# Kernel optimization log

Hardware: AMD Instinct MI355X
Metric: run time of the kernel (lower is better)

The kernel has to match this reference:

```python
import jax, jax.numpy as jnp
import numpy as np

N, E, IN, HID, HEADS, L = 50000, 640000, 32, 64, 2, 4
MAXR = 8
N_ETYPE = 11 + 3 * MAXR  # 35
NEG_SLOPE = 0.2  # DGL EGATConv leaky_relu slope


def _mlp2(x, W1, b1, W2, b2):
    # 2-layer MLP: activation (gelu) after hidden layer only
    return jax.nn.gelu(x @ W1 + b1) @ W2 + b2


def _egat(h, ef, src, dst, W_ni, W_nj, W_fij, W_node, b_node, attn):
    # DGL EGATConv: edge-feature-enhanced graph attention
    n = h.shape[0]
    H, D = attn.shape
    f_edge = (h @ W_ni)[src] + (h @ W_nj)[dst] + ef @ W_fij       # [E, H*D]
    f_out = jax.nn.leaky_relu(f_edge, NEG_SLOPE).reshape(-1, H, D)
    e = jnp.einsum('ehd,hd->eh', f_out, attn)                     # [E, H]
    m = jax.ops.segment_max(e, dst, num_segments=n)               # per-dst max
    w = jnp.exp(e - m[dst])
    z = jax.ops.segment_sum(w, dst, num_segments=n)
    a = w / z[dst]                                                # edge softmax over incoming edges
    h_out = (h @ W_node + b_node).reshape(n, H, D)
    return jax.ops.segment_sum(h_out[src] * a[:, :, None], dst, num_segments=n)  # [N, H, D]


def _forward(feat, att_rc, att_rp, type_emb, rid_emb, rc_W, rc_b, rp_W, rp_b,
             fe_W1, fe_b1, fe_W2, fe_b2, W_ni, W_nj, W_fij, W_node, b_node, attn,
             mlp_W1, mlp_b1, mlp_W2, mlp_b2, src, dst, etype, erid):
    n = feat.shape[0]
    # edge embedding, 'sum' flavor
    ef = type_emb[etype] + rid_emb[erid] + att_rc @ rc_W + rc_b + att_rp @ rp_W + rp_b
    feats = [feat]
    h = _mlp2(feat, fe_W1, fe_b1, fe_W2, fe_b2)
    feats.append(h)
    for l in range(W_ni.shape[0]):
        agg = _egat(h, ef, src, dst, W_ni[l], W_nj[l], W_fij[l],
                    W_node[l], b_node[l], attn[l])
        h = _mlp2(agg.reshape(n, -1), mlp_W1[l], mlp_b1[l], mlp_W2[l], mlp_b2[l]) + h  # residual
        feats.append(h)
    node_emb = jnp.concatenate(feats, axis=-1)             # layer_pooling='all'
    graph_emb = jnp.max(node_emb, axis=0, keepdims=True)   # graph max pooling
    return jnp.concatenate([node_emb, jnp.broadcast_to(graph_emb, node_emb.shape)], axis=-1)


def setup_inputs() -> dict:
    key = jax.random.key(0)
    ks = iter(jax.random.split(key, 40))
    s = 0.05
    return {
        'feat': jax.random.normal(next(ks), (N, IN), jnp.float32),
        'att_rc': jax.random.normal(next(ks), (E, 2), jnp.float32),
        'att_rp': jax.random.normal(next(ks), (E, 3), jnp.float32),
        'type_emb': jax.random.normal(next(ks), (N_ETYPE, HID), jnp.float32) * s,
        'rid_emb': jax.random.normal(next(ks), (MAXR + 1, HID), jnp.float32) * s,
        'rc_W': jax.random.normal(next(ks), (2, HID), jnp.float32) * s,
        'rc_b': jnp.zeros((HID,), jnp.float32),
        'rp_W': jax.random.normal(next(ks), (3, HID), jnp.float32) * s,
        'rp_b': jnp.zeros((HID,), jnp.float32),
        'fe_W1': jax.random.normal(next(ks), (IN, HID), jnp.float32) * s,
        'fe_b1': jnp.zeros((HID,), jnp.float32),
        'fe_W2': jax.random.normal(next(ks), (HID, HID), jnp.float32) * s,
        'fe_b2': jnp.zeros((HID,), jnp.float32),
        'W_ni': jax.random.normal(next(ks), (L, HID, HEADS * HID), jnp.float32) * s,
        'W_nj': jax.random.normal(next(ks), (L, HID, HEADS * HID), jnp.float32) * s,
        'W_fij': jax.random.normal(next(ks), (L, HID, HEADS * HID), jnp.float32) * s,
        'W_node': jax.random.normal(next(ks), (L, HID, HEADS * HID), jnp.float32) * s,
        'b_node': jnp.zeros((L, HEADS * HID), jnp.float32),
        'attn': jax.random.normal(next(ks), (L, HEADS, HID), jnp.float32) * s,
        'mlp_W1': jax.random.normal(next(ks), (L, HEADS * HID, HEADS * HID), jnp.float32) * s,
        'mlp_b1': jnp.zeros((L, HEADS * HID), jnp.float32),
        'mlp_W2': jax.random.normal(next(ks), (L, HEADS * HID, HID), jnp.float32) * s,
        'mlp_b2': jnp.zeros((L, HID), jnp.float32),
        'src': jax.random.randint(next(ks), (E,), 0, N, jnp.int32),
        'dst': jax.random.randint(next(ks), (E,), 0, N, jnp.int32),
        'etype': jax.random.randint(next(ks), (E,), 0, N_ETYPE, jnp.int32),
        'erid': jax.random.randint(next(ks), (E,), 0, MAXR + 1, jnp.int32),
    }


def reference(feat, att_rc, att_rp, type_emb, rid_emb, rc_W, rc_b, rp_W, rp_b,
              fe_W1, fe_b1, fe_W2, fe_b2, W_ni, W_nj, W_fij, W_node, b_node, attn,
              mlp_W1, mlp_b1, mlp_W2, mlp_b2, src, dst, etype, erid):
    return _forward(feat, att_rc, att_rp, type_emb, rid_emb, rc_W, rc_b, rp_W, rp_b,
                    fe_W1, fe_b1, fe_W2, fe_b2, W_ni, W_nj, W_fij, W_node, b_node, attn,
                    mlp_W1, mlp_b1, mlp_W2, mlp_b2, src, dst, etype, erid)
```

## Files before the change

### kernel.cpp

```cpp
#include <hip/hip_runtime.h>
#include <math.h>

#define N_NODES 50000
#define N_EDGES 640000
#define NLAYER  4
#define NPAD    50016

typedef unsigned short bf16_t;
typedef __attribute__((ext_vector_type(8))) short s16x8;
typedef __attribute__((ext_vector_type(4))) float f32x4;

__device__ __forceinline__ float gelu_f(float x) {
    return 0.5f * x * (1.0f + tanhf(0.7978845608028654f * (x + 0.044715f * x * x * x)));
}

__device__ __forceinline__ bf16_t f2bf(float f) {
    unsigned u = __float_as_uint(f);
    unsigned r = (u + 0x7FFFu + ((u >> 16) & 1u)) >> 16;
    return (bf16_t)r;
}
__device__ __forceinline__ float bf2f(bf16_t h) { return __uint_as_float(((unsigned)h) << 16); }
__device__ __forceinline__ float bfl(unsigned x) { return __uint_as_float(x << 16); }
__device__ __forceinline__ float bfh(unsigned x) { return __uint_as_float(x & 0xFFFF0000u); }

__global__ void k_zero32(unsigned* p, int n) {
    int i = blockIdx.x * 256 + threadIdx.x;
    if (i < n) p[i] = 0u;
}

__global__ void k_hist(const int* __restrict__ dst, int* __restrict__ deg) {
    int i = blockIdx.x * 256 + threadIdx.x;
    if (i < N_EDGES) atomicAdd(&deg[dst[i]], 1);
}

__global__ void k_scan1(const int* __restrict__ deg, int* __restrict__ rowptr, int* __restrict__ bsum) {
    __shared__ int sd[1024];
    int gi = blockIdx.x * 1024 + threadIdx.x;
    int v = (gi < N_NODES) ? deg[gi] : 0;
    sd[threadIdx.x] = v;
    __syncthreads();
    for (int off = 1; off < 1024; off <<= 1) {
        int t2 = (threadIdx.x >= (unsigned)off) ? sd[threadIdx.x - off] : 0;
        __syncthreads();
        sd[threadIdx.x] += t2;
        __syncthreads();
    }
    if (gi < N_NODES) rowptr[gi] = sd[threadIdx.x] - v;
    if (threadIdx.x == 1023) bsum[blockIdx.x] = sd[1023];
}

__global__ void k_scan2(const int* __restrict__ bsum, int* __restrict__ boff, int nb) {
    if (threadIdx.x == 0 && blockIdx.x == 0) {
        int run = 0;
        for (int b = 0; b < nb; b++) { boff[b] = run; run += bsum[b]; }
    }
}

__global__ void k_scan3(int* __restrict__ rowptr, const int* __restrict__ boff) {
    int gi = blockIdx.x * 1024 + threadIdx.x;
    if (gi < N_NODES) rowptr[gi] += boff[blockIdx.x];
    if (gi == 0) rowptr[N_NODES] = N_EDGES;
}

__global__ void k_copy(const int* __restrict__ a, int* __restrict__ b) {
    int i = blockIdx.x * 256 + threadIdx.x;
    if (i < N_NODES) b[i] = a[i];
}

__global__ void k_scatter(const int* __restrict__ dst, int* __restrict__ cursor, int* __restrict__ eidx) {
    int i = blockIdx.x * 256 + threadIdx.x;
    if (i < N_EDGES) {
        int p = atomicAdd(&cursor[dst[i]], 1);
        eidx[p] = i;
    }
}

__global__ void k_sortgather(
    const int* __restrict__ eidx, const int* __restrict__ src, const int* __restrict__ dst,
    const int* __restrict__ etype, const int* __restrict__ erid,
    const float* __restrict__ att_rc, const float* __restrict__ att_rp,
    int* __restrict__ src_s, int* __restrict__ dst_s,
    int* __restrict__ etype_s, int* __restrict__ erid_s,
    float* __restrict__ rc_s, float* __restrict__ rp_s)
{
    int i = blockIdx.x * 256 + threadIdx.x;
    if (i < N_EDGES) {
        int e = eidx[i];
        src_s[i] = src[e];
        dst_s[i] = dst[e];
        etype_s[i] = etype[e];
        erid_s[i] = erid[e];
        rc_s[2 * i] = att_rc[2 * e];
        rc_s[2 * i + 1] = att_rc[2 * e + 1];
        rp_s[3 * i] = att_rp[3 * e];
        rp_s[3 * i + 1] = att_rp[3 * e + 1];
        rp_s[3 * i + 2] = att_rp[3 * e + 2];
    }
}

__global__ void k_wprep(const float* __restrict__ Wfij, const float* __restrict__ Wni,
                        const float* __restrict__ Wnj, const float* __restrict__ Wnode,
                        const float* __restrict__ W1, const float* __restrict__ W2,
                        bf16_t* __restrict__ WT, bf16_t* __restrict__ W3T,
                        bf16_t* __restrict__ W1T, bf16_t* __restrict__ W2T)
{
    int idx = blockIdx.x * 256 + threadIdx.x;
    if (idx >= NLAYER * 57344) return;
    int l = idx / 57344, r = idx % 57344;
    if (r < 8192) {
        int n = r >> 6, k = r & 63;
        WT[l * 8192 + r] = f2bf(Wfij[l * 8192 + k * 128 + n]);
    } else if (r < 32768) {
        int q = r - 8192; int c = q >> 6, k = q & 63;
        const float* src = (c < 128) ? Wni : (c < 256) ? Wnj : Wnode;
        W3T[l * 24576 + q] = f2bf(src[l * 8192 + k * 128 + (c & 127)]);
    } else if (r < 49152) {
        int q = r - 32768; int n = q >> 7, k = q & 127;
        W1T[l * 16384 + q] = f2bf(W1[l * 16384 + k * 128 + n]);
    } else {
        int q = r - 49152; int j = q >> 7, k = q & 127;
        W2T[l * 8192 + q] = f2bf(W2[l * 8192 + k * 64 + j]);
    }
}

__global__ __launch_bounds__(256) void k_fe(
    const float* __restrict__ feat, const float* __restrict__ W1, const float* __restrict__ b1,
    const float* __restrict__ W2, const float* __restrict__ b2,
    float* __restrict__ h, bf16_t* __restrict__ hb, float* __restrict__ out)
{
    __shared__ float hid[4][64];
    int w = threadIdx.x >> 6, lane = threadIdx.x & 63;
    int n = blockIdx.x * 4 + w;
    float a = b1[lane];
#pragma unroll 8
    for (int k = 0; k < 32; k++) a = fmaf(feat[n * 32 + k], W1[k * 64 + lane], a);
    hid[w][lane] = gelu_f(a);
    __syncthreads();
    float o = b2[lane];
#pragma unroll 8
    for (int k = 0; k < 64; k++) o = fmaf(hid[w][k], W2[k * 64 + lane], o);
    h[n * 64 + lane] = o;
    hb[n * 64 + lane] = f2bf(o);
    out[n * 704 + 32 + lane] = o;
    if (lane < 32) out[n * 704 + lane] = feat[n * 32 + lane];
}

__global__ __launch_bounds__(256) void k_node3(
    const bf16_t* __restrict__ hb, const bf16_t* __restrict__ W3T,
    const float* __restrict__ bnode, bf16_t* __restrict__ s)
{
    __shared__ __align__(16) bf16_t hbS[32 * 72];
    const int t = threadIdx.x;
    const int wave = t >> 6, lane = t & 63, l16 = lane & 15, quad = lane >> 4;
    const int n0 = blockIdx.x * 32;
    {
        int r = t >> 3, sg = t & 7;
        *(s16x8*)(hbS + r * 72 + sg * 8) = *(const s16x8*)(hb + (size_t)(n0 + r) * 64 + sg * 8);
    }
    __syncthreads();
    const int ng = wave & 1, ch = wave >> 1;
    const s16x8 B0 = *(const s16x8*)(hbS + (ng * 16 + l16) * 72 + quad * 8);
    const s16x8 B1 = *(const s16x8*)(hbS + (ng * 16 + l16) * 72 + 32 + quad * 8);
    const int node = n0 + ng * 16 + l16;
#pragma unroll
    for (int nt = 0; nt < 12; nt++) {
        int c0 = ch * 192 + nt * 16;
        const s16x8 A0 = *(const s16x8*)(W3T + (size_t)(c0 + l16) * 64 + quad * 8);
        const s16x8 A1 = *(const s16x8*)(W3T + (size_t)(c0 + l16) * 64 + 32 + quad * 8);
        f32x4 acc = {0.f, 0.f, 0.f, 0.f};
        acc = __builtin_amdgcn_mfma_f32_16x16x32_bf16(A0, B0, acc, 0, 0, 0);
        acc = __builtin_amdgcn_mfma_f32_16x16x32_bf16(A1, B1, acc, 0, 0, 0);
        int cb = c0 + quad * 4;
        float4 bv = make_float4(0.f, 0.f, 0.f, 0.f);
        if (cb >= 256) bv = *(const float4*)(bnode + cb - 256);
        ushort4 o;
        o.x = f2bf(acc[0] + bv.x);
        o.y = f2bf(acc[1] + bv.y);
        o.z = f2bf(acc[2] + bv.z);
        o.w = f2bf(acc[3] + bv.w);
        *(ushort4*)(s + (size_t)node * 384 + cb) = o;
    }
}

__global__ __launch_bounds__(256) void k_edge(
    const bf16_t* __restrict__ s, const bf16_t* __restrict__ WT,
    const float* __restrict__ attn,
    const float* __restrict__ type_emb, const float* __restrict__ rid_emb,
    const float* __restrict__ rcW, const float* __restrict__ rcb,
    const float* __restrict__ rpW, const float* __restrict__ rpb,
    const float* __restrict__ rc_s, const float* __restrict__ rp_s,
    const int* __restrict__ etype_s, const int* __restrict__ erid_s,
    const int* __restrict__ src_s, const int* __restrict__ dst_s,
    float* __restrict__ evals)
{
    __shared__ __align__(16) bf16_t efA[32 * 72];
    __shared__ __align__(16) bf16_t SND[32 * 136];
    const int t = threadIdx.x;
    const int wave = t >> 6, lane = t & 63;
    const int l16 = lane & 15, quad = lane >> 4;
    const int eg = wave & 1, head = wave >> 1;

    s16x8 Aw[4][2];
    float4 att4[4];
#pragma unroll
    for (int mt = 0; mt < 4; mt++) {
        const bf16_t* wrow = WT + (head * 64 + mt * 16 + l16) * 64 + quad * 8;
        Aw[mt][0] = *(const s16x8*)(wrow);
        Aw[mt][1] = *(const s16x8*)(wrow + 32);
        att4[mt] = *(const float4*)(attn + head * 64 + mt * 16 + quad * 4);
    }

    for (int tile = blockIdx.x; tile < N_EDGES / 32; tile += gridDim.x) {
        const int eb = tile * 32;
        __syncthreads();
        {
            int e = t & 31, kg = (t >> 5) * 8;
            int i = eb + e;
            int et = etype_s[i] * 64, er = erid_s[i] * 64;
            float rc0 = rc_s[i * 2 + 0], rc1 = rc_s[i * 2 + 1];
            float rp0 = rp_s[i * 3 + 0], rp1 = rp_s[i * 3 + 1], rp2 = rp_s[i * 3 + 2];
            bf16_t tmp[8];
#pragma unroll
            for (int kk = 0; kk < 8; kk++) {
                int k = kg + kk;
                float v = type_emb[et + k] + rid_emb[er + k] + rcb[k] + rpb[k];
                v = fmaf(rc0, rcW[k], v);
                v = fmaf(rc1, rcW[64 + k], v);
                v = fmaf(rp0, rpW[k], v);
                v = fmaf(rp1, rpW[64 + k], v);
                v = fmaf(rp2, rpW[128 + k], v);
                tmp[kk] = f2bf(v);
            }
            *(s16x8*)(&efA[e * 72 + kg]) = *(const s16x8*)tmp;
        }
        {
#pragma unroll
            for (int j = 0; j < 2; j++) {
                int c = t * 2 + j;
                int e = c >> 4, p = c & 15;
                int i = eb + e;
                const uint4 U = *(const uint4*)(s + (size_t)src_s[i] * 384 + p * 8);
                const uint4 V = *(const uint4*)(s + (size_t)dst_s[i] * 384 + 128 + p * 8);
                bf16_t o[8];
                o[0] = f2bf(bfl(U.x) + bfl(V.x)); o[1] = f2bf(bfh(U.x) + bfh(V.x));
                o[2] = f2bf(bfl(U.y) + bfl(V.y)); o[3] = f2bf(bfh(U.y) + bfh(V.y));
                o[4] = f2bf(bfl(U.z) + bfl(V.z)); o[5] = f2bf(bfh(U.z) + bfh(V.z));
                o[6] = f2bf(bfl(U.w) + bfl(V.w)); o[7] = f2bf(bfh(U.w) + bfh(V.w));
                *(s16x8*)(&SND[e * 136 + p * 8]) = *(const s16x8*)o;
            }
        }
        __syncthreads();

        const int e = eg * 16 + l16;
        const s16x8 B0 = *(const s16x8*)(&efA[e * 72 + quad * 8]);
        const s16x8 B1 = *(const s16x8*)(&efA[e * 72 + 32 + quad * 8]);
        f32x4 acc[4];
#pragma unroll
        for (int mt = 0; mt < 4; mt++) {
            f32x4 a = {0.f, 0.f, 0.f, 0.f};
            a = __builtin_amdgcn_mfma_f32_16x16x32_bf16(Aw[mt][0], B0, a, 0, 0, 0);
            a = __builtin_amdgcn_mfma_f32_16x16x32_bf16(Aw[mt][1], B1, a, 0, 0, 0);
            acc[mt] = a;
        }

        float p = 0.f;
#pragma unroll
        for (int mt = 0; mt < 4; mt++) {
            const ushort4 sv = *(const ushort4*)(&SND[e * 136 + mt * 16 + quad * 4]);
            float f0 = acc[mt][0] + bf2f(sv.x);
            float f1 = acc[mt][1] + bf2f(sv.y);
            float f2 = acc[mt][2] + bf2f(sv.z);
            float f3 = acc[mt][3] + bf2f(sv.w);
            f0 = (f0 >= 0.f) ? f0 : 0.2f * f0;
            f1 = (f1 >= 0.f) ? f1 : 0.2f * f1;
            f2 = (f2 >= 0.f) ? f2 : 0.2f * f2;
            f3 = (f3 >= 0.f) ? f3 : 0.2f * f3;
            p = fmaf(f0, att4[mt].x, p);
            p = fmaf(f1, att4[mt].y, p);
            p = fmaf(f2, att4[mt].z, p);
            p = fmaf(f3, att4[mt].w, p);
        }
        p += __shfl_xor(p, 16);
        p += __shfl_xor(p, 32);
        if (quad == 0) evals[(eb + e) * 2 + head] = p;
    }
}

__global__ __launch_bounds__(256) void k_soft_agg(
    const int* __restrict__ rowptr, const int* __restrict__ src_s,
    const float* __restrict__ evals, const bf16_t* __restrict__ s,
    unsigned* __restrict__ aggb)
{
    int lane = threadIdx.x & 63;
    int wid = (blockIdx.x * 256 + threadIdx.x) >> 6;
    int nw = (gridDim.x * 256) >> 6;
    const int h1 = (lane >= 32) ? 1 : 0;
    const int half = lane & 31;
    for (int n = wid; n < N_NODES; n += nw) {
        int r0 = rowptr[n], r1 = rowptr[n + 1];
        unsigned* aout = aggb + (size_t)n * 64 + lane;
        if (r0 == r1) { *aout = 0u; continue; }
        float mm = -1e30f;
        for (int i = r0 + half; i < r1; i += 32) mm = fmaxf(mm, evals[2 * i + h1]);
#pragma unroll
        for (int off = 1; off < 32; off <<= 1) mm = fmaxf(mm, __shfl_xor(mm, off));
        float z = 0.f;
        for (int i = r0 + half; i < r1; i += 32) z += expf(evals[2 * i + h1] - mm);
#pragma unroll
        for (int off = 1; off < 32; off <<= 1) z += __shfl_xor(z, off);
        float rz = 1.f / z;
        float acc0 = 0.f, acc1 = 0.f;
        for (int i = r0; i < r1; i += 8) {
            int cnt = r1 - i;
            unsigned cc[8]; float ww[8];
#pragma unroll
            for (int j = 0; j < 8; j++) {
                if (j < cnt) {
                    cc[j] = *(const unsigned*)(s + (size_t)src_s[i + j] * 384 + 256 + 2 * lane);
                    ww[j] = expf(evals[2 * (i + j) + h1] - mm) * rz;
                } else { cc[j] = 0u; ww[j] = 0.f; }
            }
#pragma unroll
            for (int j = 0; j < 8; j++) {
                acc0 = fmaf(ww[j], bfl(cc[j]), acc0);
                acc1 = fmaf(ww[j], bfh(cc[j]), acc1);
            }
        }
        *aout = (unsigned)f2bf(acc0) | ((unsigned)f2bf(acc1) << 16);
    }
}

__global__ __launch_bounds__(256) void k_mlp(
    const bf16_t* __restrict__ aggb, const bf16_t* __restrict__ W1T, const float* __restrict__ b1,
    const bf16_t* __restrict__ W2T, const float* __restrict__ b2,
    const float* __restrict__ hin, float* __restrict__ hout, bf16_t* __restrict__ houtb,
    float* __restrict__ out, int col0)
{
    __shared__ __align__(16) bf16_t aggS[32 * 136];
    __shared__ __align__(16) bf16_t hidS[32 * 136];
    const int t = threadIdx.x;
    const int wave = t >> 6, lane = t & 63, l16 = lane & 15, quad = lane >> 4;
    const int n0 = blockIdx.x * 32;
    {
        int r = t >> 3, sg = t & 7;
        *(s16x8*)(aggS + r * 136 + sg * 16) =
            *(const s16x8*)(aggb + (size_t)(n0 + r) * 128 + sg * 16);
        *(s16x8*)(aggS + r * 136 + sg * 16 + 8) =
            *(const s16x8*)(aggb + (size_t)(n0 + r) * 128 + sg * 16 + 8);
    }
    __syncthreads();
    const int ng = wave & 1, nh = wave >> 1;
    const int node = n0 + ng * 16 + l16;
    {
        const bf16_t* brow = aggS + (ng * 16 + l16) * 136 + quad * 8;
        s16x8 B[4];
#pragma unroll
        for (int ks = 0; ks < 4; ks++) B[ks] = *(const s16x8*)(brow + ks * 32);
#pragma unroll
        for (int nt = 0; nt < 4; nt++) {
            int nb = nh * 64 + nt * 16;
            f32x4 acc = {0.f, 0.f, 0.f, 0.f};
#pragma unroll
            for (int ks = 0; ks < 4; ks++) {
                const s16x8 A = *(const s16x8*)(W1T + (size_t)(nb + l16) * 128 + ks * 32 + quad * 8);
                acc = __builtin_amdgcn_mfma_f32_16x16x32_bf16(A, B[ks], acc, 0, 0, 0);
            }
            const float4 bv = *(const float4*)(b1 + nb + quad * 4);
            ushort4 o;
            o.x = f2bf(gelu_f(acc[0] + bv.x));
            o.y = f2bf(gelu_f(acc[1] + bv.y));
            o.z = f2bf(gelu_f(acc[2] + bv.z));
            o.w = f2bf(gelu_f(acc[3] + bv.w));
            *(ushort4*)(hidS + (ng * 16 + l16) * 136 + nb + quad * 4) = o;
        }
    }
    __syncthreads();
    {
        const int jh = wave >> 1;
        const bf16_t* hrow = hidS + (ng * 16 + l16) * 136 + quad * 8;
        s16x8 H[4];
#pragma unroll
        for (int ks = 0; ks < 4; ks++) H[ks] = *(const s16x8*)(hrow + ks * 32);
#pragma unroll
        for (int jt = 0; jt < 2; jt++) {
            int jb = jh * 32 + jt * 16;
            f32x4 acc = {0.f, 0.f, 0.f, 0.f};
#pragma unroll
            for (int ks = 0; ks < 4; ks++) {
                const s16x8 A = *(const s16x8*)(W2T + (size_t)(jb + l16) * 128 + ks * 32 + quad * 8);
                acc = __builtin_amdgcn_mfma_f32_16x16x32_bf16(A, H[ks], acc, 0, 0, 0);
            }
            int j0 = jb + quad * 4;
            const float4 bv = *(const float4*)(b2 + j0);
            const float4 hv = *(const float4*)(hin + (size_t)node * 64 + j0);
            float4 v;
            v.x = acc[0] + bv.x + hv.x;
            v.y = acc[1] + bv.y + hv.y;
            v.z = acc[2] + bv.z + hv.z;
            v.w = acc[3] + bv.w + hv.w;
            *(float4*)(hout + (size_t)node * 64 + j0) = v;
            ushort4 ob;
            ob.x = f2bf(v.x); ob.y = f2bf(v.y); ob.z = f2bf(v.z); ob.w = f2bf(v.w);
            *(ushort4*)(houtb + (size_t)node * 64 + j0) = ob;
            if (node < N_NODES)
                *(float4*)(out + (size_t)node * 704 + col0 + j0) = v;
        }
    }
}

__device__ __forceinline__ unsigned fmap(float v) {
    unsigned u = __float_as_uint(v);
    return (u & 0x80000000u) ? ~u : (u | 0x80000000u);
}

__global__ __launch_bounds__(384) void k_colmax(const float* __restrict__ out, unsigned* __restrict__ gmax) {
    int c = threadIdx.x;
    if (c >= 352) return;
    float m = -1e30f;
    for (int n = blockIdx.x; n < N_NODES; n += gridDim.x)
        m = fmaxf(m, out[(size_t)n * 704 + c]);
    atomicMax(gmax + c, fmap(m));
}

__global__ __launch_bounds__(384) void k_bcast(const unsigned* __restrict__ gmax, float* __restrict__ out) {
    int c = threadIdx.x;
    if (c >= 352) return;
    unsigned u = gmax[c];
    u = (u & 0x80000000u) ? (u ^ 0x80000000u) : ~u;
    float v = __uint_as_float(u);
    for (int n = blockIdx.x; n < N_NODES; n += gridDim.x)
        out[(size_t)n * 704 + 352 + c] = v;
}

extern "C" void kernel_launch(void* const* d_in, const int* in_sizes, int n_in,
                              void* d_out, int out_size, void* d_ws, size_t ws_size,
                              hipStream_t stream)
{
    (void)in_sizes; (void)n_in; (void)out_size; (void)ws_size;
    const float* feat     = (const float*)d_in[0];
    const float* att_rc   = (const float*)d_in[1];
    const float* att_rp   = (const float*)d_in[2];
    const float* type_emb = (const float*)d_in[3];
    const float* rid_emb  = (const float*)d_in[4];
    const float* rc_W     = (const float*)d_in[5];
    const float* rc_b     = (const float*)d_in[6];
    const float* rp_W     = (const float*)d_in[7];
    const float* rp_b     = (const float*)d_in[8];
    const float* fe_W1    = (const float*)d_in[9];
    const float* fe_b1    = (const float*)d_in[10];
    const float* fe_W2    = (const float*)d_in[11];
    const float* fe_b2    = (const float*)d_in[12];
    const float* W_ni     = (const float*)d_in[13];
    const float* W_nj     = (const float*)d_in[14];
    const float* W_fij    = (const float*)d_in[15];
    const float* W_node   = (const float*)d_in[16];
    const float* b_node   = (const float*)d_in[17];
    const float* attn     = (const float*)d_in[18];
    const float* mlp_W1   = (const float*)d_in[19];
    const float* mlp_b1   = (const float*)d_in[20];
    const float* mlp_W2   = (const float*)d_in[21];
    const float* mlp_b2   = (const float*)d_in[22];
    const int* src   = (const int*)d_in[23];
    const int* dst   = (const int*)d_in[24];
    const int* etype = (const int*)d_in[25];
    const int* erid  = (const int*)d_in[26];
    float* out = (float*)d_out;

    char* cur = (char*)d_ws;
    auto alloc = [&](size_t bytes) { char* p = cur; cur += (bytes + 15) & ~(size_t)15; return p; };
    float* h_a    = (float*)alloc((size_t)NPAD * 64 * 4);
    float* h_b    = (float*)alloc((size_t)NPAD * 64 * 4);
    bf16_t* hb_a  = (bf16_t*)alloc((size_t)NPAD * 64 * 2);
    bf16_t* hb_b  = (bf16_t*)alloc((size_t)NPAD * 64 * 2);
    bf16_t* s     = (bf16_t*)alloc((size_t)NPAD * 384 * 2);
    float* ev     = (float*)alloc((size_t)N_EDGES * 2 * 4);
    bf16_t* aggb  = (bf16_t*)alloc((size_t)NPAD * 128 * 2);
    int* deg     = (int*)alloc((size_t)N_NODES * 4);
    int* rowptr  = (int*)alloc((size_t)(N_NODES + 1) * 4);
    int* cursor  = (int*)alloc((size_t)N_NODES * 4);
    int* eidx    = (int*)alloc((size_t)N_EDGES * 4);
    int* src_s   = (int*)alloc((size_t)N_EDGES * 4);
    int* dst_s   = (int*)alloc((size_t)N_EDGES * 4);
    int* etype_s = (int*)alloc((size_t)N_EDGES * 4);
    int* erid_s  = (int*)alloc((size_t)N_EDGES * 4);
    float* rc_s  = (float*)alloc((size_t)N_EDGES * 2 * 4);
    float* rp_s  = (float*)alloc((size_t)N_EDGES * 3 * 4);
    bf16_t* WT   = (bf16_t*)alloc((size_t)NLAYER * 128 * 64 * 2);
    bf16_t* W3T  = (bf16_t*)alloc((size_t)NLAYER * 384 * 64 * 2);
    bf16_t* W1T  = (bf16_t*)alloc((size_t)NLAYER * 128 * 128 * 2);
    bf16_t* W2T  = (bf16_t*)alloc((size_t)NLAYER * 64 * 128 * 2);
    int* bsum    = (int*)alloc(64 * 4);
    int* boff    = (int*)alloc(64 * 4);
    unsigned* gmax = (unsigned*)alloc(352 * 4);

    const int NB = (N_NODES + 1023) / 1024;

    k_zero32<<<(N_NODES + 255) / 256, 256, 0, stream>>>((unsigned*)deg, N_NODES);
    k_zero32<<<2, 256, 0, stream>>>(gmax, 352);
    k_hist<<<N_EDGES / 256, 256, 0, stream>>>(dst, deg);
    k_scan1<<<NB, 1024, 0, stream>>>(deg, rowptr, bsum);
    k_scan2<<<1, 64, 0, stream>>>(bsum, boff, NB);
    k_scan3<<<NB, 1024, 0, stream>>>(rowptr, boff);
    k_copy<<<(N_NODES + 255) / 256, 256, 0, stream>>>(rowptr, cursor);
    k_scatter<<<N_EDGES / 256, 256, 0, stream>>>(dst, cursor, eidx);
    k_sortgather<<<N_EDGES / 256, 256, 0, stream>>>(eidx, src, dst, etype, erid, att_rc, att_rp,
                                                    src_s, dst_s, etype_s, erid_s, rc_s, rp_s);
    k_wprep<<<(NLAYER * 57344 + 255) / 256, 256, 0, stream>>>(
        W_fij, W_ni, W_nj, W_node, mlp_W1, mlp_W2, WT, W3T, W1T, W2T);
    k_fe<<<N_NODES / 4, 256, 0, stream>>>(feat, fe_W1, fe_b1, fe_W2, fe_b2, h_a, hb_a, out);

    float* hc = h_a;  bf16_t* hbc = hb_a;
    float* hn = h_b;  bf16_t* hbn = hb_b;
    for (int l = 0; l < NLAYER; l++) {
        k_node3<<<NPAD / 32, 256, 0, stream>>>(hbc, W3T + (size_t)l * 384 * 64, b_node + l * 128, s);
        k_edge<<<2560, 256, 0, stream>>>(s, WT + l * 128 * 64, attn + l * 128,
                                         type_emb, rid_emb, rc_W, rc_b, rp_W, rp_b,
                                         rc_s, rp_s, etype_s, erid_s, src_s, dst_s, ev);
        k_soft_agg<<<4096, 256, 0, stream>>>(rowptr, src_s, ev, s, (unsigned*)aggb);
        k_mlp<<<NPAD / 32, 256, 0, stream>>>(aggb, W1T + (size_t)l * 128 * 128, mlp_b1 + l * 128,
                                             W2T + (size_t)l * 64 * 128, mlp_b2 + l * 64,
                                             hc, hn, hbn, out, 32 + 64 * (l + 1));
        float* tf = hc; hc = hn; hn = tf;
        bf16_t* tb = hbc; hbc = hbn; hbn = tb;
    }
    k_colmax<<<512, 384, 0, stream>>>(out, gmax);
    k_bcast<<<512, 384, 0, stream>>>(gmax, out);
}
```

Before: 1.332 ms.

## Gather node projections into registers in edge kernel, one tile per block

Measured after the change: 1.729 ms. 1.3x slower.

```diff
diff --git a/kernel.cpp b/kernel.cpp
--- a/kernel.cpp
+++ b/kernel.cpp
@@ -194,11 +194,22 @@
     float* __restrict__ evals)
 {
     __shared__ __align__(16) bf16_t efA[32 * 72];
-    __shared__ __align__(16) bf16_t SND[32 * 136];
     const int t = threadIdx.x;
     const int wave = t >> 6, lane = t & 63;
     const int l16 = lane & 15, quad = lane >> 4;
     const int eg = wave & 1, head = wave >> 1;
+    const int eb = blockIdx.x * 32;
+    const int e = eg * 16 + l16;
+    const int gi = eb + e;
+
+    const int srcn = src_s[gi], dstn = dst_s[gi];
+    ushort4 u4[4], v4[4];
+#pragma unroll
+    for (int mt = 0; mt < 4; mt++) {
+        const int c = head * 64 + mt * 16 + quad * 4;
+        u4[mt] = *(const ushort4*)(s + (size_t)srcn * 384 + c);
+        v4[mt] = *(const ushort4*)(s + (size_t)dstn * 384 + 128 + c);
+    }
 
     s16x8 Aw[4][2];
     float4 att4[4];
@@ -210,80 +221,58 @@
         att4[mt] = *(const float4*)(attn + head * 64 + mt * 16 + quad * 4);
     }
 
-    for (int tile = blockIdx.x; tile < N_EDGES / 32; tile += gridDim.x) {
-        const int eb = tile * 32;
-        __syncthreads();
-        {
-            int e = t & 31, kg = (t >> 5) * 8;
-            int i = eb + e;
-            int et = etype_s[i] * 64, er = erid_s[i] * 64;
-            float rc0 = rc_s[i * 2 + 0], rc1 = rc_s[i * 2 + 1];
-            float rp0 = rp_s[i * 3 + 0], rp1 = rp_s[i * 3 + 1], rp2 = rp_s[i * 3 + 2];
-            bf16_t tmp[8];
-#pragma unroll
-            for (int kk = 0; kk < 8; kk++) {
-                int k = kg + kk;
-                float v = type_emb[et + k] + rid_emb[er + k] + rcb[k] + rpb[k];
-                v = fmaf(rc0, rcW[k], v);
-                v = fmaf(rc1, rcW[64 + k], v);
-                v = fmaf(rp0, rpW[k], v);
-                v = fmaf(rp1, rpW[64 + k], v);
-                v = fmaf(rp2, rpW[128 + k], v);
-                tmp[kk] = f2bf(v);
-            }
-            *(s16x8*)(&efA[e * 72 + kg]) = *(const s16x8*)tmp;
+    {
+        int el = t & 31, kg = (t >> 5) * 8;
+        int i = eb + el;
+        int et = etype_s[i] * 64, er = erid_s[i] * 64;
+        float rc0 = rc_s[i * 2 + 0], rc1 = rc_s[i * 2 + 1];
+        float rp0 = rp_s[i * 3 + 0], rp1 = rp_s[i * 3 + 1], rp2 = rp_s[i * 3 + 2];
+        bf16_t tmp[8];
+#pragma unroll
+        for (int kk = 0; kk < 8; kk++) {
+            int k = kg + kk;
+            float v = type_emb[et + k] + rid_emb[er + k] + rcb[k] + rpb[k];
+            v = fmaf(rc0, rcW[k], v);
+            v = fmaf(rc1, rcW[64 + k], v);
+            v = fmaf(rp0, rpW[k], v);
+            v = fmaf(rp1, rpW[64 + k], v);
+            v = fmaf(rp2, rpW[128 + k], v);
+            tmp[kk] = f2bf(v);
         }
-        {
-#pragma unroll
-            for (int j = 0; j < 2; j++) {
-                int c = t * 2 + j;
-                int e = c >> 4, p = c & 15;
-                int i = eb + e;
-                const uint4 U = *(const uint4*)(s + (size_t)src_s[i] * 384 + p * 8);
-                const uint4 V = *(const uint4*)(s + (size_t)dst_s[i] * 384 + 128 + p * 8);
-                bf16_t o[8];
-                o[0] = f2bf(bfl(U.x) + bfl(V.x)); o[1] = f2bf(bfh(U.x) + bfh(V.x));
-                o[2] = f2bf(bfl(U.y) + bfl(V.y)); o[3] = f2bf(bfh(U.y) + bfh(V.y));
-                o[4] = f2bf(bfl(U.z) + bfl(V.z)); o[5] = f2bf(bfh(U.z) + bfh(V.z));
-                o[6] = f2bf(bfl(U.w) + bfl(V.w)); o[7] = f2bf(bfh(U.w) + bfh(V.w));
-                *(s16x8*)(&SND[e * 136 + p * 8]) = *(const s16x8*)o;
-            }
-        }
-        __syncthreads();
-
-        const int e = eg * 16 + l16;
-        const s16x8 B0 = *(const s16x8*)(&efA[e * 72 + quad * 8]);
-        const s16x8 B1 = *(const s16x8*)(&efA[e * 72 + 32 + quad * 8]);
-        f32x4 acc[4];
-#pragma unroll
-        for (int mt = 0; mt < 4; mt++) {
-            f32x4 a = {0.f, 0.f, 0.f, 0.f};
-            a = __builtin_amdgcn_mfma_f32_16x16x32_bf16(Aw[mt][0], B0, a, 0, 0, 0);
-            a = __builtin_amdgcn_mfma_f32_16x16x32_bf16(Aw[mt][1], B1, a, 0, 0, 0);
-            acc[mt] = a;
-        }
-
-        float p = 0.f;
-#pragma unroll
-        for (int mt = 0; mt < 4; mt++) {
-            const ushort4 sv = *(const ushort4*)(&SND[e * 136 + mt * 16 + quad * 4]);
-            float f0 = acc[mt][0] + bf2f(sv.x);
-            float f1 = acc[mt][1] + bf2f(sv.y);
-            float f2 = acc[mt][2] + bf2f(sv.z);
-            float f3 = acc[mt][3] + bf2f(sv.w);
-            f0 = (f0 >= 0.f) ? f0 : 0.2f * f0;
-            f1 = (f1 >= 0.f) ? f1 : 0.2f * f1;
-            f2 = (f2 >= 0.f) ? f2 : 0.2f * f2;
-            f3 = (f3 >= 0.f) ? f3 : 0.2f * f3;
-            p = fmaf(f0, att4[mt].x, p);
-            p = fmaf(f1, att4[mt].y, p);
-            p = fmaf(f2, att4[mt].z, p);
-            p = fmaf(f3, att4[mt].w, p);
-        }
-        p += __shfl_xor(p, 16);
-        p += __shfl_xor(p, 32);
-        if (quad == 0) evals[(eb + e) * 2 + head] = p;
-    }
+        *(s16x8*)(&efA[el * 72 + kg]) = *(const s16x8*)tmp;
+    }
+    __syncthreads();
+
+    const s16x8 B0 = *(const s16x8*)(&efA[e * 72 + quad * 8]);
+    const s16x8 B1 = *(const s16x8*)(&efA[e * 72 + 32 + quad * 8]);
+    f32x4 acc[4];
+#pragma unroll
+    for (int mt = 0; mt < 4; mt++) {
+        f32x4 a = {0.f, 0.f, 0.f, 0.f};
+        a = __builtin_amdgcn_mfma_f32_16x16x32_bf16(Aw[mt][0], B0, a, 0, 0, 0);
+        a = __builtin_amdgcn_mfma_f32_16x16x32_bf16(Aw[mt][1], B1, a, 0, 0, 0);
+        acc[mt] = a;
+    }
+
+    float p = 0.f;
+#pragma unroll
+    for (int mt = 0; mt < 4; mt++) {
+        float f0 = acc[mt][0] + bf2f(u4[mt].x) + bf2f(v4[mt].x);
+        float f1 = acc[mt][1] + bf2f(u4[mt].y) + bf2f(v4[mt].y);
+        float f2 = acc[mt][2] + bf2f(u4[mt].z) + bf2f(v4[mt].z);
+        float f3 = acc[mt][3] + bf2f(u4[mt].w) + bf2f(v4[mt].w);
+        f0 = (f0 >= 0.f) ? f0 : 0.2f * f0;
+        f1 = (f1 >= 0.f) ? f1 : 0.2f * f1;
+        f2 = (f2 >= 0.f) ? f2 : 0.2f * f2;
+        f3 = (f3 >= 0.f) ? f3 : 0.2f * f3;
+        p = fmaf(f0, att4[mt].x, p);
+        p = fmaf(f1, att4[mt].y, p);
+        p = fmaf(f2, att4[mt].z, p);
+        p = fmaf(f3, att4[mt].w, p);
+    }
+    p += __shfl_xor(p, 16);
+    p += __shfl_xor(p, 32);
+    if (quad == 0) evals[gi * 2 + head] = p;
 }
 
 __global__ __launch_bounds__(256) void k_soft_agg(
@@ -310,18 +299,18 @@
         for (int off = 1; off < 32; off <<= 1) z += __shfl_xor(z, off);
         float rz = 1.f / z;
         float acc0 = 0.f, acc1 = 0.f;
-        for (int i = r0; i < r1; i += 8) {
+        for (int i = r0; i < r1; i += 16) {
             int cnt = r1 - i;
-            unsigned cc[8]; float ww[8];
-#pragma unroll
-            for (int j = 0; j < 8; j++) {
+            unsigned cc[16]; float ww[16];
+#pragma unroll
+            for (int j = 0; j < 16; j++) {
                 if (j < cnt) {
                     cc[j] = *(const unsigned*)(s + (size_t)src_s[i + j] * 384 + 256 + 2 * lane);
                     ww[j] = expf(evals[2 * (i + j) + h1] - mm) * rz;
                 } else { cc[j] = 0u; ww[j] = 0.f; }
             }
 #pragma unroll
-            for (int j = 0; j < 8; j++) {
+            for (int j = 0; j < 16; j++) {
                 acc0 = fmaf(ww[j], bfl(cc[j]), acc0);
                 acc1 = fmaf(ww[j], bfh(cc[j]), acc1);
             }
@@ -513,10 +502,10 @@
     float* hn = h_b;  bf16_t* hbn = hb_b;
     for (int l = 0; l < NLAYER; l++) {
         k_node3<<<NPAD / 32, 256, 0, stream>>>(hbc, W3T + (size_t)l * 384 * 64, b_node + l * 128, s);
-        k_edge<<<2560, 256, 0, stream>>>(s, WT + l * 128 * 64, attn + l * 128,
-                                         type_emb, rid_emb, rc_W, rc_b, rp_W, rp_b,
-                                         rc_s, rp_s, etype_s, erid_s, src_s, dst_s, ev);
-        k_soft_agg<<<4096, 256, 0, stream>>>(rowptr, src_s, ev, s, (unsigned*)aggb);
+        k_edge<<<N_EDGES / 32, 256, 0, stream>>>(s, WT + l * 128 * 64, attn + l * 128,
+                                                 type_emb, rid_emb, rc_W, rc_b, rp_W, rp_b,
+                                                 rc_s, rp_s, etype_s, erid_s, src_s, dst_s, ev);
+        k_soft_agg<<<8192, 256, 0, stream>>>(rowptr, src_s, ev, s, (unsigned*)aggb);
         k_mlp<<<NPAD / 32, 256, 0, stream>>>(aggb, W1T + (size_t)l * 128 * 128, mlp_b1 + l * 128,
                                              W2T + (size_t)l * 64 * 128, mlp_b2 + l * 64,
                                              hc, hn, hbn, out, 32 + 64 * (l + 1));
```
